# Optimization experiments

Hardware: AMD Instinct MI355X
Metric: run time of the kernel (lower is better)

The kernel has to match this reference:

```python
import jax, jax.numpy as jnp
import numpy as np
from jax import lax

BN_EPS = 1e-5


def conv2d_same(x, w, b):
    # x: (B,C,H,W), w: (O,C,3,3), padding=1, stride=1
    y = lax.conv_general_dilated(x, w, window_strides=(1, 1),
                                 padding=((1, 1), (1, 1)),
                                 dimension_numbers=('NCHW', 'OIHW', 'NCHW'))
    return y + b[None, :, None, None]


def batchnorm_train(x, gamma, beta):
    # training-mode BN: biased batch statistics over (B,H,W)
    mean = jnp.mean(x, axis=(0, 2, 3), keepdims=True)
    var = jnp.var(x, axis=(0, 2, 3), keepdims=True)
    xn = (x - mean) * lax.rsqrt(var + BN_EPS)
    return xn * gamma[None, :, None, None] + beta[None, :, None, None]


def maxpool2(x):
    return lax.reduce_window(x, -jnp.inf, lax.max,
                             window_dimensions=(1, 1, 2, 2),
                             window_strides=(1, 1, 2, 2), padding='VALID')


def upsample_bilinear_align(x, scale=2):
    # matches F.interpolate(mode='bilinear', align_corners=True), then *scale
    B, C, h, w = x.shape
    oh, ow = scale * h, scale * w
    ys = jnp.arange(oh, dtype=x.dtype) * ((h - 1) / (oh - 1))
    xs = jnp.arange(ow, dtype=x.dtype) * ((w - 1) / (ow - 1))
    y0 = jnp.floor(ys).astype(jnp.int32)
    x0 = jnp.floor(xs).astype(jnp.int32)
    y1 = jnp.minimum(y0 + 1, h - 1)
    x1 = jnp.minimum(x0 + 1, w - 1)
    wy = (ys - y0.astype(x.dtype))[:, None]   # (oh,1)
    wx = (xs - x0.astype(x.dtype))[None, :]   # (1,ow)
    g = lambda yi, xi: x[:, :, yi[:, None], xi[None, :]]  # (B,C,oh,ow)
    top = g(y0, x0) * (1 - wx) + g(y0, x1) * wx
    bot = g(y1, x0) * (1 - wx) + g(y1, x1) * wx
    return scale * (top * (1 - wy) + bot * wy)


def setup_inputs() -> dict:
    key = jax.random.key(0)
    ks = jax.random.split(key, 5)
    B, C, H, W = 2, 32, 64, 64
    return {
        'X_tnext': jax.random.normal(ks[0], (B, C, H, W), jnp.float32),
        'X_hat_tnext': jax.random.normal(ks[1], (B, C, H, W), jnp.float32),
        'f_tprev_t': jax.random.normal(ks[2], (B, C, H, W), jnp.float32),
        'conv_w': jax.random.normal(ks[3], (C, C, 3, 3), jnp.float32) * 0.05,
        'conv_b': jnp.zeros((C,), jnp.float32),
        'bn_gamma': jnp.ones((C,), jnp.float32),
        'bn_beta': jnp.zeros((C,), jnp.float32),
    }


def reference(X_tnext, X_hat_tnext, f_tprev_t, conv_w, conv_b, bn_gamma, bn_beta):
    B, C, H, W = X_tnext.shape
    N = H * W
    Xv = X_tnext.reshape(B, C, N)
    Xh = X_hat_tnext.reshape(B, C, N)
    # corr4D: (B,N,N) = X^T @ Xhat / sqrt(C)
    corr = jnp.einsum('bcn,bcm->bnm', Xv, Xh) / jnp.sqrt(jnp.float32(C))
    # mat_mul[b,c,n] = sum_m corr[b,n,m] * X[b,c,m]
    mm = jnp.einsum('bnm,bcm->bcn', corr, Xv).reshape(B, C, H, W)
    x = maxpool2(jax.nn.relu(batchnorm_train(conv2d_same(mm, conv_w, conv_b), bn_gamma, bn_beta)))
    x = upsample_bilinear_align(x, scale=2)
    return x + 0.2 * f_tprev_t
```

## Files before the change

kernel.cpp:

```cpp
#include <hip/hip_runtime.h>
#include <math.h>

#define CCH  32
#define NPIX 4096
#define BB   2

__global__ __launch_bounds__(256) void k_gram(const float* __restrict__ X,
                                              const float* __restrict__ Xh,
                                              float* __restrict__ G) {
    int blk = blockIdx.x;
    int b = blk >> 10;
    int i = (blk >> 5) & 31;
    int j = blk & 31;
    const float4* xh = (const float4*)(Xh + (size_t)(b*CCH + i) * NPIX);
    const float4* xv = (const float4*)(X  + (size_t)(b*CCH + j) * NPIX);
    int t = threadIdx.x;
    float s = 0.f;
    #pragma unroll
    for (int k = 0; k < 4; ++k) {
        float4 a = xh[t + k*256];
        float4 c = xv[t + k*256];
        s += a.x*c.x + a.y*c.y + a.z*c.z + a.w*c.w;
    }
    #pragma unroll
    for (int off = 32; off > 0; off >>= 1)
        s += __shfl_down(s, off, 64);
    __shared__ float red[4];
    int lane = t & 63, wid = t >> 6;
    if (lane == 0) red[wid] = s;
    __syncthreads();
    if (t == 0) G[blk] = red[0] + red[1] + red[2] + red[3];
}

__global__ __launch_bounds__(256) void k_weff(const float* __restrict__ wConv,
                                              const float* __restrict__ G,
                                              float* __restrict__ wEff) {
    int b = blockIdx.x >> 5;
    int o = blockIdx.x & 31;
    const float rs = 0.17677669529663687f;
    for (int r = threadIdx.x; r < CCH*9; r += 256) {
        int i = r / 9, k = r - 9*(r/9);
        float s = 0.f;
        #pragma unroll 8
        for (int c = 0; c < CCH; ++c)
            s += wConv[(o*CCH + c)*9 + k] * G[(b*CCH + i)*CCH + c];
        wEff[((b*CCH + o)*CCH + i)*9 + k] = s * rs;
    }
}

__global__ __launch_bounds__(256) void k_conv(const float* __restrict__ X,
                                              const float* __restrict__ wEff,
                                              const float* __restrict__ bias,
                                              float* __restrict__ out) {
    int blk = blockIdx.x;
    int b   = blk / 512;
    int rem = blk - b*512;
    int o   = rem >> 4;
    int rt  = rem & 15;

    __shared__ float lw[CCH*9];
    const float* wsrc = wEff + (size_t)((b*CCH + o)*CCH)*9;
    for (int r = threadIdx.x; r < CCH*9; r += 256) lw[r] = wsrc[r];
    __syncthreads();

    int x = threadIdx.x & 63;
    int y = rt*4 + (threadIdx.x >> 6);
    int xl = max(x-1, 0), xr = min(x+1, 63);
    int yu = max(y-1, 0), yd = min(y+1, 63);
    float mxl = (x > 0)  ? 1.f : 0.f;
    float mxr = (x < 63) ? 1.f : 0.f;
    float myu = (y > 0)  ? 1.f : 0.f;
    float myd = (y < 63) ? 1.f : 0.f;
    float m0 = myu*mxl, m1 = myu, m2 = myu*mxr;
    float m3 = mxl,               m5 = mxr;
    float m6 = myd*mxl, m7 = myd, m8 = myd*mxr;

    const float* plane = X + (size_t)b*CCH*NPIX;
    int ou = yu*64, o0 = y*64, od = yd*64;
    float acc = bias[o];
    #pragma unroll 4
    for (int i = 0; i < CCH; ++i) {
        const float* p   = plane + i*NPIX;
        const float* lwi = lw + i*9;
        float v0 = p[ou + xl] * m0;
        float v1 = p[ou + x ] * m1;
        float v2 = p[ou + xr] * m2;
        float v3 = p[o0 + xl] * m3;
        float v4 = p[o0 + x ];
        float v5 = p[o0 + xr] * m5;
        float v6 = p[od + xl] * m6;
        float v7 = p[od + x ] * m7;
        float v8 = p[od + xr] * m8;
        acc = fmaf(lwi[0], v0, acc);
        acc = fmaf(lwi[1], v1, acc);
        acc = fmaf(lwi[2], v2, acc);
        acc = fmaf(lwi[3], v3, acc);
        acc = fmaf(lwi[4], v4, acc);
        acc = fmaf(lwi[5], v5, acc);
        acc = fmaf(lwi[6], v6, acc);
        acc = fmaf(lwi[7], v7, acc);
        acc = fmaf(lwi[8], v8, acc);
    }
    out[(size_t)(b*CCH + o)*NPIX + y*64 + x] = acc;
}

__global__ __launch_bounds__(256) void k_stats(const float* __restrict__ conv_out,
                                               const float* __restrict__ gamma,
                                               const float* __restrict__ beta,
                                               float* __restrict__ ss) {
    int c = blockIdx.x;
    double s = 0.0, s2 = 0.0;
    for (int b = 0; b < BB; ++b) {
        const float4* p = (const float4*)(conv_out + (size_t)(b*CCH + c)*NPIX);
        for (int k = threadIdx.x; k < NPIX/4; k += 256) {
            float4 v = p[k];
            s  += (double)v.x + (double)v.y + (double)v.z + (double)v.w;
            s2 += (double)v.x*v.x + (double)v.y*v.y + (double)v.z*v.z + (double)v.w*v.w;
        }
    }
    #pragma unroll
    for (int off = 32; off > 0; off >>= 1) {
        s  += __shfl_down(s,  off, 64);
        s2 += __shfl_down(s2, off, 64);
    }
    __shared__ double rs[4], rs2[4];
    int lane = threadIdx.x & 63, wid = threadIdx.x >> 6;
    if (lane == 0) { rs[wid] = s; rs2[wid] = s2; }
    __syncthreads();
    if (threadIdx.x == 0) {
        double S  = rs[0] + rs[1] + rs[2] + rs[3];
        double S2 = rs2[0] + rs2[1] + rs2[2] + rs2[3];
        double n    = (double)(BB * NPIX);
        double mean = S / n;
        double var  = S2 / n - mean*mean;
        float invstd = (float)(1.0 / sqrt(var + 1e-5));
        float sc = gamma[c] * invstd;
        float sh = beta[c] - (float)mean * sc;
        ss[c]      = sc;
        ss[32 + c] = sh;
    }
}

__global__ __launch_bounds__(256) void k_tail(const float* __restrict__ conv_out,
                                              const float* __restrict__ ss,
                                              const float* __restrict__ f,
                                              float* __restrict__ out) {
    int b = blockIdx.x >> 5;
    int c = blockIdx.x & 31;
    float sc = ss[c];
    float sh = ss[32 + c];
    const float* plane = conv_out + (size_t)(b*CCH + c)*NPIX;
    __shared__ float pool[32*32];
    int t = threadIdx.x;
    #pragma unroll
    for (int q = 0; q < 4; ++q) {
        int idx = t + q*256;
        int py = idx >> 5, px = idx & 31;
        float2 a = *(const float2*)(plane + (2*py)*64   + 2*px);
        float2 d = *(const float2*)(plane + (2*py+1)*64 + 2*px);
        float v0 = fmaxf(fmaf(a.x, sc, sh), 0.f);
        float v1 = fmaxf(fmaf(a.y, sc, sh), 0.f);
        float v2 = fmaxf(fmaf(d.x, sc, sh), 0.f);
        float v3 = fmaxf(fmaf(d.y, sc, sh), 0.f);
        pool[idx] = fmaxf(fmaxf(v0, v1), fmaxf(v2, v3));
    }
    __syncthreads();
    const float r = 31.f / 63.f;
    const float* fp = f   + (size_t)(b*CCH + c)*NPIX;
    float*       op = out + (size_t)(b*CCH + c)*NPIX;
    #pragma unroll
    for (int q = 0; q < 16; ++q) {
        int idx = t + q*256;
        int oy = idx >> 6, ox = idx & 63;
        float ysf = (float)oy * r;
        float xsf = (float)ox * r;
        int y0 = (int)ysf;
        int x0 = (int)xsf;
        float wy = ysf - (float)y0;
        float wx = xsf - (float)x0;
        int y1 = min(y0 + 1, 31);
        int x1 = min(x0 + 1, 31);
        float p00 = pool[y0*32 + x0];
        float p01 = pool[y0*32 + x1];
        float p10 = pool[y1*32 + x0];
        float p11 = pool[y1*32 + x1];
        float top = p00 + (p01 - p00) * wx;
        float bot = p10 + (p11 - p10) * wx;
        float val = 2.f * (top + (bot - top) * wy);
        op[idx] = val + 0.2f * fp[idx];
    }
}

extern "C" void kernel_launch(void* const* d_in, const int* in_sizes, int n_in,
                              void* d_out, int out_size, void* d_ws, size_t ws_size,
                              hipStream_t stream) {
    const float* X   = (const float*)d_in[0];
    const float* Xh  = (const float*)d_in[1];
    const float* f   = (const float*)d_in[2];
    const float* wC  = (const float*)d_in[3];
    const float* bC  = (const float*)d_in[4];
    const float* gam = (const float*)d_in[5];
    const float* bet = (const float*)d_in[6];
    float* out = (float*)d_out;

    float* W     = (float*)d_ws;
    float* G     = W;
    float* wEff  = W + 2048;
    float* ss    = W + 20480;
    float* convo = W + 20544;

    hipLaunchKernelGGL(k_gram,  dim3(2048), dim3(256), 0, stream, X, Xh, G);
    hipLaunchKernelGGL(k_weff,  dim3(64),   dim3(256), 0, stream, wC, G, wEff);
    hipLaunchKernelGGL(k_conv,  dim3(1024), dim3(256), 0, stream, X, wEff, bC, convo);
    hipLaunchKernelGGL(k_stats, dim3(32),   dim3(256), 0, stream, convo, gam, bet, ss);
    hipLaunchKernelGGL(k_tail,  dim3(64),   dim3(256), 0, stream, convo, ss, f, out);
}
```

Measured before the change: 94.44 us.

## Fuse gram+weff, fold BN stats and pooling into conv epilogue

```diff
diff --git a/kernel.cpp b/kernel.cpp
--- a/kernel.cpp
+++ b/kernel.cpp
@@ -5,53 +5,61 @@
 #define NPIX 4096
 #define BB   2
 
-__global__ __launch_bounds__(256) void k_gram(const float* __restrict__ X,
-                                              const float* __restrict__ Xh,
-                                              float* __restrict__ G) {
+__global__ __launch_bounds__(256) void k_gram_weff(const float* __restrict__ X,
+                                                   const float* __restrict__ Xh,
+                                                   const float* __restrict__ wConv,
+                                                   float* __restrict__ wEff,
+                                                   float* __restrict__ sums) {
     int blk = blockIdx.x;
-    int b = blk >> 10;
-    int i = (blk >> 5) & 31;
-    int j = blk & 31;
-    const float4* xh = (const float4*)(Xh + (size_t)(b*CCH + i) * NPIX);
-    const float4* xv = (const float4*)(X  + (size_t)(b*CCH + j) * NPIX);
+    int b = blk >> 5, i = blk & 31;
     int t = threadIdx.x;
-    float s = 0.f;
-    #pragma unroll
-    for (int k = 0; k < 4; ++k) {
-        float4 a = xh[t + k*256];
-        float4 c = xv[t + k*256];
-        s += a.x*c.x + a.y*c.y + a.z*c.z + a.w*c.w;
-    }
-    #pragma unroll
-    for (int off = 32; off > 0; off >>= 1)
-        s += __shfl_down(s, off, 64);
-    __shared__ float red[4];
-    int lane = t & 63, wid = t >> 6;
-    if (lane == 0) red[wid] = s;
-    __syncthreads();
-    if (t == 0) G[blk] = red[0] + red[1] + red[2] + red[3];
-}
-
-__global__ __launch_bounds__(256) void k_weff(const float* __restrict__ wConv,
-                                              const float* __restrict__ G,
-                                              float* __restrict__ wEff) {
-    int b = blockIdx.x >> 5;
-    int o = blockIdx.x & 31;
-    const float rs = 0.17677669529663687f;
-    for (int r = threadIdx.x; r < CCH*9; r += 256) {
-        int i = r / 9, k = r - 9*(r/9);
-        float s = 0.f;
-        #pragma unroll 8
-        for (int c = 0; c < CCH; ++c)
-            s += wConv[(o*CCH + c)*9 + k] * G[(b*CCH + i)*CCH + c];
-        wEff[((b*CCH + o)*CCH + i)*9 + k] = s * rs;
+
+    if (blk == 0 && t < 64) sums[t] = 0.f;
+
+    __shared__ float xh_lds[NPIX];
+    {
+        float4* dst = (float4*)xh_lds;
+        const float4* src = (const float4*)(Xh + (size_t)(b*CCH + i) * NPIX);
+        #pragma unroll
+        for (int k = 0; k < 4; ++k) dst[t + k*256] = src[t + k*256];
+    }
+    __syncthreads();
+
+    int c = t >> 3;
+    int s = t & 7;
+    const float4* xc = (const float4*)(X + (size_t)(b*CCH + c) * NPIX);
+    const float4* xh4 = (const float4*)xh_lds;
+    float acc = 0.f;
+    #pragma unroll 8
+    for (int k = 0; k < 128; ++k) {
+        float4 v = xc[s + k*8];
+        float4 h = xh4[s + k*8];
+        acc += v.x*h.x + v.y*h.y + v.z*h.z + v.w*h.w;
+    }
+    acc += __shfl_down(acc, 4, 8);
+    acc += __shfl_down(acc, 2, 8);
+    acc += __shfl_down(acc, 1, 8);
+
+    __shared__ float g[CCH];
+    if (s == 0) g[c] = acc;
+    __syncthreads();
+
+    for (int r = t; r < CCH*9; r += 256) {
+        int o = r / 9, k = r - 9*(r/9);
+        float sacc = 0.f;
+        #pragma unroll
+        for (int cc = 0; cc < CCH; ++cc)
+            sacc += wConv[(o*CCH + cc)*9 + k] * g[cc];
+        wEff[((b*CCH + o)*CCH + i)*9 + k] = sacc * 0.17677669529663687f;
     }
 }
 
 __global__ __launch_bounds__(256) void k_conv(const float* __restrict__ X,
                                               const float* __restrict__ wEff,
                                               const float* __restrict__ bias,
-                                              float* __restrict__ out) {
+                                              float* __restrict__ poolMax,
+                                              float* __restrict__ poolMin,
+                                              float* __restrict__ sums) {
     int blk = blockIdx.x;
     int b   = blk / 512;
     int rem = blk - b*512;
@@ -101,70 +109,66 @@
         acc = fmaf(lwi[7], v7, acc);
         acc = fmaf(lwi[8], v8, acc);
     }
-    out[(size_t)(b*CCH + o)*NPIX + y*64 + x] = acc;
-}
-
-__global__ __launch_bounds__(256) void k_stats(const float* __restrict__ conv_out,
-                                               const float* __restrict__ gamma,
-                                               const float* __restrict__ beta,
-                                               float* __restrict__ ss) {
-    int c = blockIdx.x;
-    double s = 0.0, s2 = 0.0;
-    for (int b = 0; b < BB; ++b) {
-        const float4* p = (const float4*)(conv_out + (size_t)(b*CCH + c)*NPIX);
-        for (int k = threadIdx.x; k < NPIX/4; k += 256) {
-            float4 v = p[k];
-            s  += (double)v.x + (double)v.y + (double)v.z + (double)v.w;
-            s2 += (double)v.x*v.x + (double)v.y*v.y + (double)v.z*v.z + (double)v.w*v.w;
-        }
-    }
+
+    __shared__ float tile[256];
+    tile[threadIdx.x] = acc;
+
+    float s1 = acc, s2 = acc*acc;
     #pragma unroll
     for (int off = 32; off > 0; off >>= 1) {
-        s  += __shfl_down(s,  off, 64);
+        s1 += __shfl_down(s1, off, 64);
         s2 += __shfl_down(s2, off, 64);
     }
-    __shared__ double rs[4], rs2[4];
+    __shared__ float r1[4], r2[4];
     int lane = threadIdx.x & 63, wid = threadIdx.x >> 6;
-    if (lane == 0) { rs[wid] = s; rs2[wid] = s2; }
+    if (lane == 0) { r1[wid] = s1; r2[wid] = s2; }
     __syncthreads();
     if (threadIdx.x == 0) {
-        double S  = rs[0] + rs[1] + rs[2] + rs[3];
-        double S2 = rs2[0] + rs2[1] + rs2[2] + rs2[3];
-        double n    = (double)(BB * NPIX);
-        double mean = S / n;
-        double var  = S2 / n - mean*mean;
-        float invstd = (float)(1.0 / sqrt(var + 1e-5));
-        float sc = gamma[c] * invstd;
-        float sh = beta[c] - (float)mean * sc;
-        ss[c]      = sc;
-        ss[32 + c] = sh;
-    }
-}
-
-__global__ __launch_bounds__(256) void k_tail(const float* __restrict__ conv_out,
-                                              const float* __restrict__ ss,
+        atomicAdd(&sums[o],      r1[0] + r1[1] + r1[2] + r1[3]);
+        atomicAdd(&sums[32 + o], r2[0] + r2[1] + r2[2] + r2[3]);
+    }
+
+    if (threadIdx.x < 64) {
+        int py = threadIdx.x >> 5;
+        int px = threadIdx.x & 31;
+        const float* row0 = &tile[(2*py)*64 + 2*px];
+        const float* row1 = &tile[(2*py+1)*64 + 2*px];
+        float a0 = row0[0], a1 = row0[1], b0 = row1[0], b1 = row1[1];
+        float mx = fmaxf(fmaxf(a0, a1), fmaxf(b0, b1));
+        float mn = fminf(fminf(a0, a1), fminf(b0, b1));
+        size_t pidx = (size_t)(b*CCH + o)*1024 + (rt*2 + py)*32 + px;
+        poolMax[pidx] = mx;
+        poolMin[pidx] = mn;
+    }
+}
+
+__global__ __launch_bounds__(256) void k_tail(const float* __restrict__ poolMax,
+                                              const float* __restrict__ poolMin,
+                                              const float* __restrict__ sums,
+                                              const float* __restrict__ gamma,
+                                              const float* __restrict__ beta,
                                               const float* __restrict__ f,
                                               float* __restrict__ out) {
     int b = blockIdx.x >> 5;
     int c = blockIdx.x & 31;
-    float sc = ss[c];
-    float sh = ss[32 + c];
-    const float* plane = conv_out + (size_t)(b*CCH + c)*NPIX;
-    __shared__ float pool[32*32];
+    float S  = sums[c];
+    float S2 = sums[32 + c];
+    const float invN = 1.f / (BB * NPIX);
+    float mean = S * invN;
+    float var  = S2 * invN - mean*mean;
+    float sc = gamma[c] / sqrtf(var + 1e-5f);
+    float sh = beta[c] - mean * sc;
+
+    const float* psel = (sc >= 0.f ? poolMax : poolMin) + (size_t)(b*CCH + c)*1024;
+    __shared__ float pool[1024];
     int t = threadIdx.x;
     #pragma unroll
     for (int q = 0; q < 4; ++q) {
         int idx = t + q*256;
-        int py = idx >> 5, px = idx & 31;
-        float2 a = *(const float2*)(plane + (2*py)*64   + 2*px);
-        float2 d = *(const float2*)(plane + (2*py+1)*64 + 2*px);
-        float v0 = fmaxf(fmaf(a.x, sc, sh), 0.f);
-        float v1 = fmaxf(fmaf(a.y, sc, sh), 0.f);
-        float v2 = fmaxf(fmaf(d.x, sc, sh), 0.f);
-        float v3 = fmaxf(fmaf(d.y, sc, sh), 0.f);
-        pool[idx] = fmaxf(fmaxf(v0, v1), fmaxf(v2, v3));
-    }
-    __syncthreads();
+        pool[idx] = fmaxf(fmaf(psel[idx], sc, sh), 0.f);
+    }
+    __syncthreads();
+
     const float r = 31.f / 63.f;
     const float* fp = f   + (size_t)(b*CCH + c)*NPIX;
     float*       op = out + (size_t)(b*CCH + c)*NPIX;
@@ -203,15 +207,13 @@
     const float* bet = (const float*)d_in[6];
     float* out = (float*)d_out;
 
-    float* W     = (float*)d_ws;
-    float* G     = W;
-    float* wEff  = W + 2048;
-    float* ss    = W + 20480;
-    float* convo = W + 20544;
-
-    hipLaunchKernelGGL(k_gram,  dim3(2048), dim3(256), 0, stream, X, Xh, G);
-    hipLaunchKernelGGL(k_weff,  dim3(64),   dim3(256), 0, stream, wC, G, wEff);
-    hipLaunchKernelGGL(k_conv,  dim3(1024), dim3(256), 0, stream, X, wEff, bC, convo);
-    hipLaunchKernelGGL(k_stats, dim3(32),   dim3(256), 0, stream, convo, gam, bet, ss);
-    hipLaunchKernelGGL(k_tail,  dim3(64),   dim3(256), 0, stream, convo, ss, f, out);
-}
+    float* W       = (float*)d_ws;
+    float* wEff    = W;
+    float* sums    = W + 18432;
+    float* poolMax = W + 18496;
+    float* poolMin = W + 84032;
+
+    hipLaunchKernelGGL(k_gram_weff, dim3(64),   dim3(256), 0, stream, X, Xh, wC, wEff, sums);
+    hipLaunchKernelGGL(k_conv,      dim3(1024), dim3(256), 0, stream, X, wEff, bC, poolMax, poolMin, sums);
+    hipLaunchKernelGGL(k_tail,      dim3(64),   dim3(256), 0, stream, poolMax, poolMin, sums, gam, bet, f, out);
+}
```

New measurement: 100.2 us. +6.1%, slower.
